# Kernel optimization log

Measured on AMD Instinct MI355X. Metric: run time of the kernel, lower is better.

Reference implementation:

```python
import jax, jax.numpy as jnp
import numpy as np
from jax import lax

DILATIONS = [1, 2, 4, 8, 16, 32, 64, 128, 256, 512]
L = len(DILATIONS)
T = 2048          # input_size (== sequence length)
C = 128           # residual channels
COND = 16         # condition vector dim
B = 8


def conv1d(x, w, dilation=1):
    # x: [B, T, Cin], w: [K, Cin, Cout] (WIO), SAME padding like keras Conv1D
    return lax.conv_general_dilated(
        x, w, window_strides=(1,), padding='SAME',
        rhs_dilation=(dilation,), dimension_numbers=('NWC', 'WIO', 'NWC'))


def setup_inputs() -> dict:
    key = jax.random.key(0)
    ks = iter(jax.random.split(key, 32))
    n = lambda shape, s=0.05: jax.random.normal(next(ks), shape, dtype=jnp.float32) * s
    inp = {
        'x': jax.random.normal(next(ks), (B, T, 1), dtype=jnp.float32),
        'condition': jax.random.normal(next(ks), (B, COND), dtype=jnp.float32),
        # input projection Conv1D(128, 1)
        'Wc': n((1, 1, C)), 'bc': jnp.zeros((C,), jnp.float32),
        # per-block dilated gated convs Conv1D(128, 3), stacked over L blocks
        'Wt': n((L, 3, C, C)), 'bt': jnp.zeros((L, C), jnp.float32),
        'Ws': n((L, 3, C, C)), 'bs': jnp.zeros((L, C), jnp.float32),
        # stacked conditioning Dense weights: 128 Dense(cond->T) per branch per block
        # Dense i weight [COND, T]; stacked & transposed -> [L, COND, T, 128]
        'Dt': n((L, COND, T, C)), 'Bt': jnp.zeros((L, T, C), jnp.float32),
        'Ds': n((L, COND, T, C)), 'Bs': jnp.zeros((L, T, C), jnp.float32),
        # skip / residual 1x1 convs
        'Wskip': n((L, 1, C, C)), 'bskip': jnp.zeros((L, C), jnp.float32),
        'Wres': n((L, 1, C, C)), 'bres': jnp.zeros((L, C), jnp.float32),
        # output head
        'W1': n((3, C, 2048)), 'b1': jnp.zeros((2048,), jnp.float32),
        'W2': n((3, 2048, 256)), 'b2': jnp.zeros((256,), jnp.float32),
        'W3': n((1, 256, 1)), 'b3': jnp.zeros((1,), jnp.float32),
    }
    return inp


def reference(x, condition, Wc, bc, Wt, bt, Ws, bs, Dt, Bt, Ds, Bs,
              Wskip, bskip, Wres, bres, W1, b1, W2, b2, W3, b3):
    h = conv1d(x, Wc) + bc  # [B, T, 128]
    skip_sum = jnp.zeros_like(h)
    for l, d in enumerate(DILATIONS):
        # fused equivalent of 128 per-channel Dense layers + concat:
        # trans[b,t,k] = condition[b,:] @ Dense_k.W + Dense_k.b
        tt = jnp.einsum('bc,ctk->btk', condition, Dt[l]) + Bt[l]
        ts = jnp.einsum('bc,ctk->btk', condition, Ds[l]) + Bs[l]
        g = jnp.tanh(conv1d(h, Wt[l], d) + bt[l] + tt) * \
            jax.nn.sigmoid(conv1d(h, Ws[l], d) + bs[l] + ts)
        skip_sum = skip_sum + conv1d(g, Wskip[l]) + bskip[l]
        h = conv1d(g, Wres[l]) + bres[l] + h
    out = jax.nn.relu(conv1d(skip_sum, W1) + b1)  # [B, T, 2048]
    out = jax.nn.relu(conv1d(out, W2) + b2)       # [B, T, 256]
    out = jnp.tanh(conv1d(out, W3) + b3)          # [B, T, 1]
    return out
```

## Files before the change

kernel.cpp:

```cpp
#include <hip/hip_runtime.h>
#include <hip/hip_bf16.h>
#include <math.h>

#define T 2048
#define C 128
#define BATCH 8
#define NLAYER 10

typedef short bf16x8 __attribute__((ext_vector_type(8)));
typedef float f32x4 __attribute__((ext_vector_type(4)));
typedef unsigned short u16x4 __attribute__((ext_vector_type(4)));

__device__ __forceinline__ float sigmoidf_(float x) {
    return 1.f / (1.f + __expf(-x));
}
__device__ __forceinline__ float tanhf_(float x) {
    float a = fabsf(x);
    float e = __expf(-2.f * a);
    float t = (1.f - e) / (1.f + e);
    return copysignf(t, x);
}
__device__ __forceinline__ ushort f2bf(float v) {
    __hip_bfloat16 h = __float2bfloat16(v);
    return *reinterpret_cast<ushort*>(&h);
}
__device__ __forceinline__ float bf2f(ushort u) {
    unsigned int x = ((unsigned int)u) << 16;
    return __uint_as_float(x);
}
__device__ __forceinline__ void gl_lds16(const ushort* g, ushort* l) {
    __builtin_amdgcn_global_load_lds(
        (const __attribute__((address_space(1))) unsigned int*)g,
        (__attribute__((address_space(3))) unsigned int*)l, 16, 0, 0);
}

__global__ void k_init(const float* __restrict__ x, const float* __restrict__ Wc,
                       const float* __restrict__ bc, float* __restrict__ h32,
                       ushort* __restrict__ hb, float* __restrict__ skip) {
    int i = blockIdx.x * 256 + threadIdx.x;
    int c = i & 127;
    int pos = i >> 7;
    float v = x[pos] * Wc[c] + bc[c];
    h32[i] = v;
    hb[i] = f2bf(v);
    skip[i] = 0.f;
}

__global__ void k_prep_wg(const float* __restrict__ Wt, const float* __restrict__ Ws,
                          ushort* __restrict__ WGb) {
    int n = blockIdx.x;
    int l = blockIdx.y;
    int t = threadIdx.x;
    int j = t >> 7, ci = t & 127;
    const float* src = (n < 128) ? Wt : Ws;
    int col = n & 127;
    WGb[((size_t)(l * 256 + n)) * 384 + t] = f2bf(src[(((size_t)l * 3 + j) * 128 + ci) * 128 + col]);
}
__global__ void k_prep_wr(const float* __restrict__ Wskip, const float* __restrict__ Wres,
                          ushort* __restrict__ WRb) {
    int n = blockIdx.x;
    int l = blockIdx.y;
    int ci = threadIdx.x;
    const float* src = (n < 128) ? Wskip : Wres;
    int col = n & 127;
    WRb[((size_t)(l * 256 + n)) * 128 + ci] = f2bf(src[((size_t)l * 128 + ci) * 128 + col]);
}
template<int KIN>
__global__ void k_prep_w(const float* __restrict__ W, ushort* __restrict__ Wb, int N) {
    int n = blockIdx.x;
    for (int k = threadIdx.x; k < 3 * KIN; k += blockDim.x)
        Wb[(size_t)n * (3 * KIN) + k] = f2bf(W[(size_t)k * N + n]);
}
__global__ void k_f32_to_bf16(const float* __restrict__ in, ushort* __restrict__ out, int n) {
    int i = blockIdx.x * 256 + threadIdx.x;
    if (i < n) out[i] = f2bf(in[i]);
}
__global__ void k_zero_pad(ushort* __restrict__ out1p) {
    int i = blockIdx.x * 256 + threadIdx.x;
    int ri = i >> 10, col = i & 1023;
    int b = ri >> 1, pr = (ri & 1) ? 2049 : 0;
    ((unsigned int*)out1p)[((size_t)b * 2050 + pr) * 1024 + col] = 0u;
}

__global__ __launch_bounds__(256) void k_cond(
    const float* __restrict__ cond,
    const float* __restrict__ Dt, const float* __restrict__ Bt,
    const float* __restrict__ Ds, const float* __restrict__ Bs,
    const float* __restrict__ bt, const float* __restrict__ bs,
    ushort* __restrict__ z0, int l0)
{
    const int l  = l0 + blockIdx.y;
    const int ll = blockIdx.y;
    const int k4 = (threadIdx.x & 31) * 4;
    const int tq = threadIdx.x >> 5;
    const int t  = blockIdx.x * 8 + tq;

    __shared__ float sc[128];
    if (threadIdx.x < 128) sc[threadIdx.x] = cond[threadIdx.x];
    __syncthreads();

    const f32x4 btv = *(const f32x4*)(bt + l * 128 + k4);
    const f32x4 bsv = *(const f32x4*)(bs + l * 128 + k4);
    const f32x4 Btv = *(const f32x4*)(Bt + ((size_t)l * T + t) * 128 + k4);
    const f32x4 Bsv = *(const f32x4*)(Bs + ((size_t)l * T + t) * 128 + k4);

    f32x4 zt[8], zs[8];
    #pragma unroll
    for (int b = 0; b < 8; ++b) {
        zt[b] = btv + Btv;
        zs[b] = bsv + Bsv;
    }

    const float* dtp = Dt + (((size_t)l * 16) * T + t) * 128 + k4;
    const float* dsp = Ds + (((size_t)l * 16) * T + t) * 128 + k4;
    #pragma unroll
    for (int c = 0; c < 16; ++c) {
        const f32x4 dv = *(const f32x4*)(dtp + (size_t)c * T * 128);
        const f32x4 sv = *(const f32x4*)(dsp + (size_t)c * T * 128);
        #pragma unroll
        for (int b = 0; b < 8; ++b) {
            const float cb = sc[b * 16 + c];
            zt[b] += cb * dv;
            zs[b] += cb * sv;
        }
    }

    #pragma unroll
    for (int b = 0; b < 8; ++b) {
        size_t zb = (((size_t)ll * 8 + b) * T + t) * 256;
        u16x4 pt, ps;
        #pragma unroll
        for (int j = 0; j < 4; ++j) {
            pt[j] = f2bf(zt[b][j]);
            ps[j] = f2bf(zs[b][j]);
        }
        *(u16x4*)(z0 + zb + k4)       = pt;
        *(u16x4*)(z0 + zb + 128 + k4) = ps;
    }
}

__global__ __launch_bounds__(256) void k_gate(
    const float* __restrict__ h32_in, float* __restrict__ h32_out,
    const ushort* __restrict__ hb_in, ushort* __restrict__ hb_out,
    float* __restrict__ skip32,
    const ushort* __restrict__ WG,
    const ushort* __restrict__ WR,
    const ushort* __restrict__ z0l,
    const float* __restrict__ bskip, const float* __restrict__ bres,
    int d)
{
    __shared__ ushort lds[3 * 32 * 136];
    const int tid  = threadIdx.x;
    const int lane = tid & 63, ln16 = lane & 15, quad = lane >> 4;
    const int wave = tid >> 6;
    const int n_off = wave * 64;
    const int t0 = blockIdx.x * 4;

    #pragma unroll
    for (int it = 0; it < 6; ++it) {
        int task = tid + it * 256;
        int part = task & 15;
        int r = (task >> 4) & 31;
        int j = task >> 9;
        int t = t0 + (r >> 3) + (j - 1) * d;
        int b = r & 7;
        uint4 v = make_uint4(0u, 0u, 0u, 0u);
        if (t >= 0 && t < T) v = *(const uint4*)(hb_in + ((size_t)b * T + t) * 128 + part * 8);
        *(uint4*)(&lds[(j * 32 + r) * 136 + part * 8]) = v;
    }
    __syncthreads();

    f32x4 acc[2][4];
    #pragma unroll
    for (int mt = 0; mt < 2; ++mt)
        #pragma unroll
        for (int nt = 0; nt < 4; ++nt)
            acc[mt][nt] = (f32x4){0.f, 0.f, 0.f, 0.f};

    #pragma unroll
    for (int j = 0; j < 3; ++j) {
        #pragma unroll
        for (int kc = 0; kc < 4; ++kc) {
            bf16x8 af[2], bfr[4];
            #pragma unroll
            for (int mt = 0; mt < 2; ++mt)
                af[mt] = *(const bf16x8*)(&lds[(j * 32 + mt * 16 + ln16) * 136 + kc * 32 + quad * 8]);
            #pragma unroll
            for (int nt = 0; nt < 4; ++nt)
                bfr[nt] = *(const bf16x8*)(WG + (size_t)(n_off + nt * 16 + ln16) * 384 + j * 128 + kc * 32 + quad * 8);
            #pragma unroll
            for (int mt = 0; mt < 2; ++mt)
                #pragma unroll
                for (int nt = 0; nt < 4; ++nt)
                    acc[mt][nt] = __builtin_amdgcn_mfma_f32_16x16x32_bf16(af[mt], bfr[nt], acc[mt][nt], 0, 0, 0);
        }
    }
    __syncthreads();

    #pragma unroll
    for (int mt = 0; mt < 2; ++mt) {
        #pragma unroll
        for (int nt = 0; nt < 4; ++nt) {
            int n = n_off + nt * 16 + ln16;
            #pragma unroll
            for (int r4 = 0; r4 < 4; ++r4) {
                int row = mt * 16 + quad * 4 + r4;
                int b = row & 7, p = row >> 3;
                float z = acc[mt][nt][r4] + bf2f(z0l[((size_t)b * T + t0 + p) * 256 + n]);
                lds[row * 264 + n] = f2bf(z);
            }
        }
    }
    __syncthreads();

    {
        int r = tid >> 3;
        int k0 = (tid & 7) * 16;
        #pragma unroll
        for (int kk = 0; kk < 16; ++kk) {
            int k = k0 + kk;
            float zt = bf2f(lds[r * 264 + k]);
            float zs = bf2f(lds[r * 264 + 128 + k]);
            lds[8704 + r * 136 + k] = f2bf(tanhf_(zt) * sigmoidf_(zs));
        }
    }
    __syncthreads();

    f32x4 acc2[2][4];
    #pragma unroll
    for (int mt = 0; mt < 2; ++mt)
        #pragma unroll
        for (int nt = 0; nt < 4; ++nt)
            acc2[mt][nt] = (f32x4){0.f, 0.f, 0.f, 0.f};

    #pragma unroll
    for (int kc = 0; kc < 4; ++kc) {
        bf16x8 af[2], bfr[4];
        #pragma unroll
        for (int mt = 0; mt < 2; ++mt)
            af[mt] = *(const bf16x8*)(&lds[8704 + (mt * 16 + ln16) * 136 + kc * 32 + quad * 8]);
        #pragma unroll
        for (int nt = 0; nt < 4; ++nt)
            bfr[nt] = *(const bf16x8*)(WR + (size_t)(n_off + nt * 16 + ln16) * 128 + kc * 32 + quad * 8);
        #pragma unroll
        for (int mt = 0; mt < 2; ++mt)
            #pragma unroll
            for (int nt = 0; nt < 4; ++nt)
                acc2[mt][nt] = __builtin_amdgcn_mfma_f32_16x16x32_bf16(af[mt], bfr[nt], acc2[mt][nt], 0, 0, 0);
    }

    #pragma unroll
    for (int mt = 0; mt < 2; ++mt) {
        #pragma unroll
        for (int nt = 0; nt < 4; ++nt) {
            int n = n_off + nt * 16 + ln16;
            int k = n & 127;
            #pragma unroll
            for (int r4 = 0; r4 < 4; ++r4) {
                int row = mt * 16 + quad * 4 + r4;
                int b = row & 7, p = row >> 3;
                size_t idx = ((size_t)b * T + t0 + p) * 128 + k;
                float v = acc2[mt][nt][r4];
                if (n < 128) {
                    skip32[idx] += v + bskip[k];
                } else {
                    float hv = v + bres[k] + h32_in[idx];
                    h32_out[idx] = hv;
                    hb_out[idx] = f2bf(hv);
                }
            }
        }
    }
}

template<int KIN, bool OUT_BF16>
__global__ __launch_bounds__(256) void k_conv_mfma(
    const ushort* __restrict__ A, const ushort* __restrict__ Wb,
    const float* __restrict__ bias, void* __restrict__ outv,
    int b_in_off, int b_out_off, int ots, int oto)
{
    constexpr int AS = 40;
    __shared__ ushort As[66 * AS];
    __shared__ ushort Bs[3 * 128 * AS];

    const int tid  = threadIdx.x;
    const int lane = tid & 63;
    const int ln16 = lane & 15;
    const int quad = lane >> 4;
    const int wave = tid >> 6;
    const int m_off = (wave & 1) * 32;
    const int n_off = (wave >> 1) * 64;

    const int t0 = blockIdx.x * 64;
    const int n0 = blockIdx.y * 128;
    const int bz = blockIdx.z;
    const int N  = gridDim.y * 128;

    const ushort* Ab = A + (size_t)(b_in_off + bz) * T * KIN;

    f32x4 acc[2][4];
    #pragma unroll
    for (int mi = 0; mi < 2; ++mi)
        #pragma unroll
        for (int ni = 0; ni < 4; ++ni)
            acc[mi][ni] = (f32x4){0.f, 0.f, 0.f, 0.f};

    for (int cc = 0; cc < KIN / 32; ++cc) {
        for (int idx = tid; idx < 66 * 4; idx += 256) {
            int r = idx >> 2, part = idx & 3;
            int t = t0 - 1 + r;
            uint4 v = make_uint4(0u, 0u, 0u, 0u);
            if (t >= 0 && t < T)
                v = *(const uint4*)(Ab + (size_t)t * KIN + cc * 32 + part * 8);
            *(uint4*)(&As[r * AS + part * 8]) = v;
        }
        #pragma unroll
        for (int it = 0; it < 6; ++it) {
            int idx = tid + it * 256;
            int jr = idx >> 2, part = idx & 3;
            int j = jr >> 7, n = jr & 127;
            uint4 v = *(const uint4*)(Wb + (size_t)(n0 + n) * (3 * KIN) + j * KIN + cc * 32 + part * 8);
            *(uint4*)(&Bs[jr * AS + part * 8]) = v;
        }
        __syncthreads();

        #pragma unroll
        for (int j = 0; j < 3; ++j) {
            bf16x8 af[2], bf[4];
            #pragma unroll
            for (int mi = 0; mi < 2; ++mi)
                af[mi] = *(const bf16x8*)(&As[(m_off + mi * 16 + ln16 + j) * AS + quad * 8]);
            #pragma unroll
            for (int ni = 0; ni < 4; ++ni)
                bf[ni] = *(const bf16x8*)(&Bs[(j * 128 + n_off + ni * 16 + ln16) * AS + quad * 8]);
            #pragma unroll
            for (int mi = 0; mi < 2; ++mi)
                #pragma unroll
                for (int ni = 0; ni < 4; ++ni)
                    acc[mi][ni] = __builtin_amdgcn_mfma_f32_16x16x32_bf16(af[mi], bf[ni], acc[mi][ni], 0, 0, 0);
        }
        __syncthreads();
    }

    #pragma unroll
    for (int ni = 0; ni < 4; ++ni) {
        int n = n0 + n_off + ni * 16 + ln16;
        float bv = bias[n];
        #pragma unroll
        for (int mi = 0; mi < 2; ++mi) {
            #pragma unroll
            for (int r = 0; r < 4; ++r) {
                int m = m_off + mi * 16 + quad * 4 + r;
                int t = t0 + m;
                float v = fmaxf(acc[mi][ni][r] + bv, 0.f);
                size_t oi = ((size_t)(b_out_off + bz) * ots + oto + t) * N + n;
                if constexpr (OUT_BF16) ((ushort*)outv)[oi] = f2bf(v);
                else                    ((float*)outv)[oi]  = v;
            }
        }
    }
}

#define CV2_AUS 8704
#define CV2_BUS 24576
#define CV2_BUF 33280

__global__ __launch_bounds__(256) void k_conv2t(
    const ushort* __restrict__ A,
    const ushort* __restrict__ Wb,
    const float* __restrict__ bias,
    float* __restrict__ out2)
{
    __shared__ ushort sh[2 * CV2_BUF];
    const int tid  = threadIdx.x;
    const int lane = tid & 63, ln16 = lane & 15, quad = lane >> 4;
    const int wave = tid >> 6;
    const int wm = wave >> 1, wn = wave & 1;
    const int m0 = blockIdx.x * 128;
    const int b  = blockIdx.y;
    const int n0 = blockIdx.z * 128;
    const size_t aRow0 = (size_t)b * 2050 + m0;

    f32x4 acc[4][4];
    #pragma unroll
    for (int i = 0; i < 4; ++i)
        #pragma unroll
        for (int j = 0; j < 4; ++j) acc[i][j] = (f32x4){0.f, 0.f, 0.f, 0.f};

    auto stage = [&](int d, int cc) {
        const int sb = d * CV2_BUF;
        const int k0 = cc * 64;
        #pragma unroll
        for (int ps = 0; ps < 4; ++ps) {
            int task = ps * 256 + tid;
            int r = task >> 3, p = task & 7, q = p ^ (r & 7);
            gl_lds16(A + (aRow0 + r) * 2048 + k0 + q * 8,
                     &sh[sb + ((ps * 256 + wave * 64) << 3)]);
        }
        if (tid < 64) {
            int task = 1024 + tid;
            int r = task >> 3, p = task & 7, q = p ^ (r & 7);
            gl_lds16(A + (aRow0 + r) * 2048 + k0 + q * 8,
                     &sh[sb + (1024 << 3)]);
        }
        #pragma unroll
        for (int ps = 0; ps < 12; ++ps) {
            int task = ps * 256 + tid;
            int rb = task >> 3, p = task & 7, q = p ^ (rb & 7);
            int nl = rb & 127, tap = rb >> 7;
            gl_lds16(Wb + (size_t)(n0 + nl) * 6144 + tap * 2048 + k0 + q * 8,
                     &sh[sb + CV2_AUS + ((ps * 256 + wave * 64) << 3)]);
        }
    };

    stage(0, 0);
    __syncthreads();

    for (int cc = 0; cc < 32; ++cc) {
        if (cc < 31) stage((cc + 1) & 1, cc + 1);
        const int sb = (cc & 1) * CV2_BUF;
        #pragma unroll
        for (int j = 0; j < 3; ++j) {
            #pragma unroll
            for (int kk = 0; kk < 2; ++kk) {
                bf16x8 af[4], bfr[4];
                #pragma unroll
                for (int mt = 0; mt < 4; ++mt) {
                    int r = wm * 64 + mt * 16 + ln16 + j;
                    int s = (kk << 2) | quad;
                    af[mt] = *(const bf16x8*)(&sh[sb + r * 64 + ((s ^ (r & 7)) << 3)]);
                }
                #pragma unroll
                for (int nt = 0; nt < 4; ++nt) {
                    int rb = j * 128 + wn * 64 + nt * 16 + ln16;
                    int s = (kk << 2) | quad;
                    bfr[nt] = *(const bf16x8*)(&sh[sb + CV2_AUS + rb * 64 + ((s ^ (rb & 7)) << 3)]);
                }
                #pragma unroll
                for (int mt = 0; mt < 4; ++mt)
                    #pragma unroll
                    for (int nt = 0; nt < 4; ++nt)
                        acc[mt][nt] = __builtin_amdgcn_mfma_f32_16x16x32_bf16(af[mt], bfr[nt], acc[mt][nt], 0, 0, 0);
            }
        }
        __syncthreads();
    }

    #pragma unroll
    for (int nt = 0; nt < 4; ++nt) {
        int n = n0 + wn * 64 + nt * 16 + ln16;
        float bv = bias[n];
        #pragma unroll
        for (int mt = 0; mt < 4; ++mt) {
            #pragma unroll
            for (int r4 = 0; r4 < 4; ++r4) {
                int m = wm * 64 + mt * 16 + quad * 4 + r4;
                int t = m0 + m;
                float v = fmaxf(acc[mt][nt][r4] + bv, 0.f);
                out2[((size_t)b * T + t) * 256 + n] = v;
            }
        }
    }
}

__global__ __launch_bounds__(256) void k_conv3(
    const float* __restrict__ out2, const float* __restrict__ W3,
    const float* __restrict__ b3, float* __restrict__ out)
{
    int wid = threadIdx.x >> 6, lane = threadIdx.x & 63;
    int pos = blockIdx.x * 4 + wid;
    float4 v = *(const float4*)(out2 + (size_t)pos * 256 + lane * 4);
    float4 w = *(const float4*)(W3 + lane * 4);
    float sum = v.x * w.x + v.y * w.y + v.z * w.z + v.w * w.w;
    #pragma unroll
    for (int off = 32; off > 0; off >>= 1) sum += __shfl_down(sum, off);
    if (lane == 0) out[pos] = tanhf_(sum + b3[0]);
}

extern "C" void kernel_launch(void* const* d_in, const int* in_sizes, int n_in,
                              void* d_out, int out_size, void* d_ws, size_t ws_size,
                              hipStream_t stream)
{
    const float* x     = (const float*)d_in[0];
    const float* cond  = (const float*)d_in[1];
    const float* Wc    = (const float*)d_in[2];
    const float* bc    = (const float*)d_in[3];
    const float* Wt    = (const float*)d_in[4];
    const float* bt    = (const float*)d_in[5];
    const float* Ws    = (const float*)d_in[6];
    const float* bs    = (const float*)d_in[7];
    const float* Dt    = (const float*)d_in[8];
    const float* Bt    = (const float*)d_in[9];
    const float* Ds    = (const float*)d_in[10];
    const float* Bs    = (const float*)d_in[11];
    const float* Wskip = (const float*)d_in[12];
    const float* bskip = (const float*)d_in[13];
    const float* Wres  = (const float*)d_in[14];
    const float* bres  = (const float*)d_in[15];
    const float* W1    = (const float*)d_in[16];
    const float* b1    = (const float*)d_in[17];
    const float* W2    = (const float*)d_in[18];
    const float* b2    = (const float*)d_in[19];
    const float* W3    = (const float*)d_in[20];
    const float* b3    = (const float*)d_in[21];
    float* out = (float*)d_out;

    float* ws = (float*)d_ws;
    float*  skip32 = ws;
    float*  h32a   = ws + 2097152;
    float*  h32b   = ws + 4194304;
    float*  out2   = ws + 6291456;
    ushort* u      = (ushort*)(ws + 10485760);
    ushort* hba    = u;
    ushort* hbb    = u + 2097152;
    ushort* WGb    = u + 4194304;
    ushort* WRb    = u + 5177344;
    ushort* W1b    = u + 5505024;
    ushort* W2b    = u + 6291456;
    ushort* skipb  = u;
    ushort* z0     = u + 9961472;
    ushort* out1p  = u + 7864320;

    k_init<<<8192, 256, 0, stream>>>(x, Wc, bc, h32a, hba, skip32);
    k_prep_wg<<<dim3(256, NLAYER), 384, 0, stream>>>(Wt, Ws, WGb);
    k_prep_wr<<<dim3(256, NLAYER), 128, 0, stream>>>(Wskip, Wres, WRb);
    k_prep_w<128><<<2048, 384, 0, stream>>>(W1, W1b, 2048);
    k_prep_w<2048><<<256, 1024, 0, stream>>>(W2, W2b, 256);

    static const int DIL[NLAYER] = {1, 2, 4, 8, 16, 32, 64, 128, 256, 512};
    float*  h32in = h32a;  float*  h32out = h32b;
    ushort* hbin  = hba;   ushort* hbout  = hbb;

    for (int chunk = 0; chunk < 2; ++chunk) {
        int l0 = chunk * 5;
        k_cond<<<dim3(T / 8, 5), 256, 0, stream>>>(cond, Dt, Bt, Ds, Bs, bt, bs, z0, l0);
        for (int l = l0; l < l0 + 5; ++l) {
            k_gate<<<512, 256, 0, stream>>>(
                h32in, h32out, hbin, hbout, skip32,
                WGb + (size_t)l * 256 * 384,
                WRb + (size_t)l * 256 * 128,
                z0 + (size_t)(l - l0) * 8 * T * 256,
                bskip + l * 128, bres + l * 128,
                DIL[l]);
            float* tf = h32in; h32in = h32out; h32out = tf;
            ushort* tu = hbin; hbin = hbout; hbout = tu;
        }
    }

    k_f32_to_bf16<<<(BATCH * T * C + 255) / 256, 256, 0, stream>>>(skip32, skipb, BATCH * T * C);
    k_zero_pad<<<64, 256, 0, stream>>>(out1p);
    k_conv_mfma<128, true><<<dim3(T / 64, 16, BATCH), 256, 0, stream>>>(
        skipb, W1b, b1, out1p, 0, 0, 2050, 1);
    k_conv2t<<<dim3(16, 8, 2), 256, 0, stream>>>(out1p, W2b, b2, out2);
    k_conv3<<<(BATCH * T) / 4, 256, 0, stream>>>(out2, W3, b3, out);
}
```

Baseline: 867.8 us.

## Tile weight prep transposes, split cond branches, rewrite conv1 with padded LDS-staged MFMA

Weight-prep kernels now transpose through 32x32 shared-memory tiles, so both global reads and writes are coalesced instead of strided. k_cond is split over a grid z-dimension into one block per branch (t/s), halving per-thread work and raising parallelism. The first head conv is replaced by a 128x128-tile MFMA kernel that reads a zero-padded skip buffer through direct global-to-LDS loads with XOR swizzle and double buffering, mirroring the conv2 kernel. Padding removes the boundary checks, at the cost of an extra padded layout and larger LDS use per block.

```diff
diff --git a/kernel.cpp b/kernel.cpp
--- a/kernel.cpp
+++ b/kernel.cpp
@@ -46,40 +46,72 @@
     skip[i] = 0.f;
 }
 
-__global__ void k_prep_wg(const float* __restrict__ Wt, const float* __restrict__ Ws,
-                          ushort* __restrict__ WGb) {
-    int n = blockIdx.x;
-    int l = blockIdx.y;
-    int t = threadIdx.x;
-    int j = t >> 7, ci = t & 127;
-    const float* src = (n < 128) ? Wt : Ws;
-    int col = n & 127;
-    WGb[((size_t)(l * 256 + n)) * 384 + t] = f2bf(src[(((size_t)l * 3 + j) * 128 + ci) * 128 + col]);
-}
-__global__ void k_prep_wr(const float* __restrict__ Wskip, const float* __restrict__ Wres,
-                          ushort* __restrict__ WRb) {
-    int n = blockIdx.x;
-    int l = blockIdx.y;
-    int ci = threadIdx.x;
-    const float* src = (n < 128) ? Wskip : Wres;
-    int col = n & 127;
-    WRb[((size_t)(l * 256 + n)) * 128 + ci] = f2bf(src[((size_t)l * 128 + ci) * 128 + col]);
-}
-template<int KIN>
-__global__ void k_prep_w(const float* __restrict__ W, ushort* __restrict__ Wb, int N) {
-    int n = blockIdx.x;
-    for (int k = threadIdx.x; k < 3 * KIN; k += blockDim.x)
-        Wb[(size_t)n * (3 * KIN) + k] = f2bf(W[(size_t)k * N + n]);
-}
-__global__ void k_f32_to_bf16(const float* __restrict__ in, ushort* __restrict__ out, int n) {
+__global__ void k_prep_wgT(const float* __restrict__ Wt, const float* __restrict__ Ws,
+                           ushort* __restrict__ WGb) {
+    const int tx = threadIdx.x, ty = threadIdx.y;
+    const int z = blockIdx.z, s = z & 1, lj = z >> 1;
+    const int l = lj / 3, j = lj % 3;
+    const float* src = (s ? Ws : Wt) + (size_t)lj * 128 * 128;
+    const int col0 = blockIdx.x * 32, ci0 = blockIdx.y * 32;
+    __shared__ float tile[32][33];
+    #pragma unroll
+    for (int i = 0; i < 4; ++i)
+        tile[ty + i * 8][tx] = src[(size_t)(ci0 + ty + i * 8) * 128 + col0 + tx];
+    __syncthreads();
+    #pragma unroll
+    for (int i = 0; i < 4; ++i)
+        WGb[((size_t)l * 256 + s * 128 + col0 + ty + i * 8) * 384 + j * 128 + ci0 + tx] =
+            f2bf(tile[tx][ty + i * 8]);
+}
+__global__ void k_prep_wrT(const float* __restrict__ Wskip, const float* __restrict__ Wres,
+                           ushort* __restrict__ WRb) {
+    const int tx = threadIdx.x, ty = threadIdx.y;
+    const int z = blockIdx.z, s = z & 1, l = z >> 1;
+    const float* src = (s ? Wres : Wskip) + (size_t)l * 128 * 128;
+    const int col0 = blockIdx.x * 32, ci0 = blockIdx.y * 32;
+    __shared__ float tile[32][33];
+    #pragma unroll
+    for (int i = 0; i < 4; ++i)
+        tile[ty + i * 8][tx] = src[(size_t)(ci0 + ty + i * 8) * 128 + col0 + tx];
+    __syncthreads();
+    #pragma unroll
+    for (int i = 0; i < 4; ++i)
+        WRb[((size_t)l * 256 + s * 128 + col0 + ty + i * 8) * 128 + ci0 + tx] =
+            f2bf(tile[tx][ty + i * 8]);
+}
+template<int R>
+__global__ void k_prep_wT(const float* __restrict__ W, ushort* __restrict__ Wb, int N) {
+    const int tx = threadIdx.x, ty = threadIdx.y;
+    const int x = blockIdx.x * 32 + tx;
+    const int y0 = blockIdx.y * 32;
+    __shared__ float tile[32][33];
+    #pragma unroll
+    for (int i = 0; i < 4; ++i)
+        tile[ty + i * 8][tx] = W[(size_t)(y0 + ty + i * 8) * N + x];
+    __syncthreads();
+    const int n0 = blockIdx.x * 32;
+    #pragma unroll
+    for (int i = 0; i < 4; ++i)
+        Wb[(size_t)(n0 + ty + i * 8) * R + y0 + tx] = f2bf(tile[tx][ty + i * 8]);
+}
+
+__global__ void k_skip_pad(const float* __restrict__ in, ushort* __restrict__ skipp) {
     int i = blockIdx.x * 256 + threadIdx.x;
-    if (i < n) out[i] = f2bf(in[i]);
-}
-__global__ void k_zero_pad(ushort* __restrict__ out1p) {
+    int b = i >> 18, rem = i & 262143;
+    skipp[(size_t)b * 262400 + 128 + rem] = f2bf(in[i]);
+}
+__global__ void k_zero_pads(ushort* __restrict__ out1p, ushort* __restrict__ skipp) {
     int i = blockIdx.x * 256 + threadIdx.x;
-    int ri = i >> 10, col = i & 1023;
-    int b = ri >> 1, pr = (ri & 1) ? 2049 : 0;
-    ((unsigned int*)out1p)[((size_t)b * 2050 + pr) * 1024 + col] = 0u;
+    if (i < 16384) {
+        int ri = i >> 10, col = i & 1023;
+        int b = ri >> 1, pr = (ri & 1) ? 2049 : 0;
+        ((unsigned int*)out1p)[((size_t)b * 2050 + pr) * 1024 + col] = 0u;
+    } else {
+        int j = i - 16384;
+        int ri = j >> 6, col = j & 63;
+        int b = ri >> 1, pr = (ri & 1) ? 2049 : 0;
+        ((unsigned int*)skipp)[((size_t)b * 2050 + pr) * 64 + col] = 0u;
+    }
 }
 
 __global__ __launch_bounds__(256) void k_cond(
@@ -89,6 +121,10 @@
     const float* __restrict__ bt, const float* __restrict__ bs,
     ushort* __restrict__ z0, int l0)
 {
+    const int br = blockIdx.z;
+    const float* D  = br ? Ds : Dt;
+    const float* B_ = br ? Bs : Bt;
+    const float* b_ = br ? bs : bt;
     const int l  = l0 + blockIdx.y;
     const int ll = blockIdx.y;
     const int k4 = (threadIdx.x & 31) * 4;
@@ -99,43 +135,29 @@
     if (threadIdx.x < 128) sc[threadIdx.x] = cond[threadIdx.x];
     __syncthreads();
 
-    const f32x4 btv = *(const f32x4*)(bt + l * 128 + k4);
-    const f32x4 bsv = *(const f32x4*)(bs + l * 128 + k4);
-    const f32x4 Btv = *(const f32x4*)(Bt + ((size_t)l * T + t) * 128 + k4);
-    const f32x4 Bsv = *(const f32x4*)(Bs + ((size_t)l * T + t) * 128 + k4);
-
-    f32x4 zt[8], zs[8];
-    #pragma unroll
-    for (int b = 0; b < 8; ++b) {
-        zt[b] = btv + Btv;
-        zs[b] = bsv + Bsv;
-    }
-
-    const float* dtp = Dt + (((size_t)l * 16) * T + t) * 128 + k4;
-    const float* dsp = Ds + (((size_t)l * 16) * T + t) * 128 + k4;
+    const f32x4 bv = *(const f32x4*)(b_ + l * 128 + k4);
+    const f32x4 Bv = *(const f32x4*)(B_ + ((size_t)l * T + t) * 128 + k4);
+
+    f32x4 z[8];
+    #pragma unroll
+    for (int b = 0; b < 8; ++b) z[b] = bv + Bv;
+
+    const float* dp = D + (((size_t)l * 16) * T + t) * 128 + k4;
     #pragma unroll
     for (int c = 0; c < 16; ++c) {
-        const f32x4 dv = *(const f32x4*)(dtp + (size_t)c * T * 128);
-        const f32x4 sv = *(const f32x4*)(dsp + (size_t)c * T * 128);
-        #pragma unroll
-        for (int b = 0; b < 8; ++b) {
-            const float cb = sc[b * 16 + c];
-            zt[b] += cb * dv;
-            zs[b] += cb * sv;
-        }
+        const f32x4 dv = *(const f32x4*)(dp + (size_t)c * T * 128);
+        #pragma unroll
+        for (int b = 0; b < 8; ++b)
+            z[b] += sc[b * 16 + c] * dv;
     }
 
     #pragma unroll
     for (int b = 0; b < 8; ++b) {
         size_t zb = (((size_t)ll * 8 + b) * T + t) * 256;
-        u16x4 pt, ps;
-        #pragma unroll
-        for (int j = 0; j < 4; ++j) {
-            pt[j] = f2bf(zt[b][j]);
-            ps[j] = f2bf(zs[b][j]);
-        }
-        *(u16x4*)(z0 + zb + k4)       = pt;
-        *(u16x4*)(z0 + zb + 128 + k4) = ps;
+        u16x4 p;
+        #pragma unroll
+        for (int j = 0; j < 4; ++j) p[j] = f2bf(z[b][j]);
+        *(u16x4*)(z0 + zb + br * 128 + k4) = p;
     }
 }
 
@@ -273,97 +295,106 @@
     }
 }
 
-template<int KIN, bool OUT_BF16>
-__global__ __launch_bounds__(256) void k_conv_mfma(
-    const ushort* __restrict__ A, const ushort* __restrict__ Wb,
-    const float* __restrict__ bias, void* __restrict__ outv,
-    int b_in_off, int b_out_off, int ots, int oto)
+#define CV2_AUS 8704
+#define CV2_BUF 33280
+
+__global__ __launch_bounds__(256) void k_conv1t(
+    const ushort* __restrict__ A,
+    const ushort* __restrict__ Wb,
+    const float* __restrict__ bias,
+    ushort* __restrict__ out1p)
 {
-    constexpr int AS = 40;
-    __shared__ ushort As[66 * AS];
-    __shared__ ushort Bs[3 * 128 * AS];
-
+    __shared__ ushort sh[2 * CV2_BUF];
     const int tid  = threadIdx.x;
-    const int lane = tid & 63;
-    const int ln16 = lane & 15;
-    const int quad = lane >> 4;
+    const int lane = tid & 63, ln16 = lane & 15, quad = lane >> 4;
     const int wave = tid >> 6;
-    const int m_off = (wave & 1) * 32;
-    const int n_off = (wave >> 1) * 64;
-
-    const int t0 = blockIdx.x * 64;
-    const int n0 = blockIdx.y * 128;
-    const int bz = blockIdx.z;
-    const int N  = gridDim.y * 128;
-
-    const ushort* Ab = A + (size_t)(b_in_off + bz) * T * KIN;
-
-    f32x4 acc[2][4];
-    #pragma unroll
-    for (int mi = 0; mi < 2; ++mi)
-        #pragma unroll
-        for (int ni = 0; ni < 4; ++ni)
-            acc[mi][ni] = (f32x4){0.f, 0.f, 0.f, 0.f};
-
-    for (int cc = 0; cc < KIN / 32; ++cc) {
-        for (int idx = tid; idx < 66 * 4; idx += 256) {
-            int r = idx >> 2, part = idx & 3;
-            int t = t0 - 1 + r;
-            uint4 v = make_uint4(0u, 0u, 0u, 0u);
-            if (t >= 0 && t < T)
-                v = *(const uint4*)(Ab + (size_t)t * KIN + cc * 32 + part * 8);
-            *(uint4*)(&As[r * AS + part * 8]) = v;
-        }
-        #pragma unroll
-        for (int it = 0; it < 6; ++it) {
-            int idx = tid + it * 256;
-            int jr = idx >> 2, part = idx & 3;
-            int j = jr >> 7, n = jr & 127;
-            uint4 v = *(const uint4*)(Wb + (size_t)(n0 + n) * (3 * KIN) + j * KIN + cc * 32 + part * 8);
-            *(uint4*)(&Bs[jr * AS + part * 8]) = v;
+    const int wm = wave >> 1, wn = wave & 1;
+    const int m0 = blockIdx.x * 128;
+    const int b  = blockIdx.y;
+    const int n0 = blockIdx.z * 128;
+    const size_t aRow0 = (size_t)b * 2050 + m0;
+
+    f32x4 acc[4][4];
+    #pragma unroll
+    for (int i = 0; i < 4; ++i)
+        #pragma unroll
+        for (int j = 0; j < 4; ++j) acc[i][j] = (f32x4){0.f, 0.f, 0.f, 0.f};
+
+    auto stage = [&](int d, int c) {
+        const int sb = d * CV2_BUF;
+        const int k0 = c * 64;
+        #pragma unroll
+        for (int ps = 0; ps < 4; ++ps) {
+            int task = ps * 256 + tid;
+            int r = task >> 3, p = task & 7, q = p ^ (r & 7);
+            gl_lds16(A + (aRow0 + r) * 128 + k0 + q * 8,
+                     &sh[sb + ((ps * 256 + wave * 64) << 3)]);
+        }
+        if (tid < 64) {
+            int task = 1024 + tid;
+            int r = task >> 3, p = task & 7, q = p ^ (r & 7);
+            gl_lds16(A + (aRow0 + r) * 128 + k0 + q * 8,
+                     &sh[sb + (1024 << 3)]);
+        }
+        #pragma unroll
+        for (int ps = 0; ps < 12; ++ps) {
+            int task = ps * 256 + tid;
+            int rb = task >> 3, p = task & 7, q = p ^ (rb & 7);
+            int nl = rb & 127, tap = rb >> 7;
+            gl_lds16(Wb + (size_t)(n0 + nl) * 384 + tap * 128 + k0 + q * 8,
+                     &sh[sb + CV2_AUS + ((ps * 256 + wave * 64) << 3)]);
+        }
+    };
+
+    stage(0, 0);
+    __syncthreads();
+
+    for (int c = 0; c < 2; ++c) {
+        if (c == 0) stage(1, 1);
+        const int sb = (c & 1) * CV2_BUF;
+        #pragma unroll
+        for (int j = 0; j < 3; ++j) {
+            #pragma unroll
+            for (int kk = 0; kk < 2; ++kk) {
+                bf16x8 af[4], bfr[4];
+                #pragma unroll
+                for (int mt = 0; mt < 4; ++mt) {
+                    int r = wm * 64 + mt * 16 + ln16 + j;
+                    int s = (kk << 2) | quad;
+                    af[mt] = *(const bf16x8*)(&sh[sb + r * 64 + ((s ^ (r & 7)) << 3)]);
+                }
+                #pragma unroll
+                for (int nt = 0; nt < 4; ++nt) {
+                    int rb = j * 128 + wn * 64 + nt * 16 + ln16;
+                    int s = (kk << 2) | quad;
+                    bfr[nt] = *(const bf16x8*)(&sh[sb + CV2_AUS + rb * 64 + ((s ^ (rb & 7)) << 3)]);
+                }
+                #pragma unroll
+                for (int mt = 0; mt < 4; ++mt)
+                    #pragma unroll
+                    for (int nt = 0; nt < 4; ++nt)
+                        acc[mt][nt] = __builtin_amdgcn_mfma_f32_16x16x32_bf16(af[mt], bfr[nt], acc[mt][nt], 0, 0, 0);
+            }
         }
         __syncthreads();
-
-        #pragma unroll
-        for (int j = 0; j < 3; ++j) {
-            bf16x8 af[2], bf[4];
-            #pragma unroll
-            for (int mi = 0; mi < 2; ++mi)
-                af[mi] = *(const bf16x8*)(&As[(m_off + mi * 16 + ln16 + j) * AS + quad * 8]);
-            #pragma unroll
-            for (int ni = 0; ni < 4; ++ni)
-                bf[ni] = *(const bf16x8*)(&Bs[(j * 128 + n_off + ni * 16 + ln16) * AS + quad * 8]);
-            #pragma unroll
-            for (int mi = 0; mi < 2; ++mi)
-                #pragma unroll
-                for (int ni = 0; ni < 4; ++ni)
-                    acc[mi][ni] = __builtin_amdgcn_mfma_f32_16x16x32_bf16(af[mi], bf[ni], acc[mi][ni], 0, 0, 0);
-        }
-        __syncthreads();
-    }
-
-    #pragma unroll
-    for (int ni = 0; ni < 4; ++ni) {
-        int n = n0 + n_off + ni * 16 + ln16;
+    }
+
+    #pragma unroll
+    for (int nt = 0; nt < 4; ++nt) {
+        int n = n0 + wn * 64 + nt * 16 + ln16;
         float bv = bias[n];
         #pragma unroll
-        for (int mi = 0; mi < 2; ++mi) {
-            #pragma unroll
-            for (int r = 0; r < 4; ++r) {
-                int m = m_off + mi * 16 + quad * 4 + r;
-                int t = t0 + m;
-                float v = fmaxf(acc[mi][ni][r] + bv, 0.f);
-                size_t oi = ((size_t)(b_out_off + bz) * ots + oto + t) * N + n;
-                if constexpr (OUT_BF16) ((ushort*)outv)[oi] = f2bf(v);
-                else                    ((float*)outv)[oi]  = v;
+        for (int mt = 0; mt < 4; ++mt) {
+            #pragma unroll
+            for (int r4 = 0; r4 < 4; ++r4) {
+                int m = wm * 64 + mt * 16 + quad * 4 + r4;
+                int t = m0 + m;
+                float v = fmaxf(acc[mt][nt][r4] + bv, 0.f);
+                out1p[((size_t)b * 2050 + 1 + t) * 2048 + n] = f2bf(v);
             }
         }
     }
 }
-
-#define CV2_AUS 8704
-#define CV2_BUS 24576
-#define CV2_BUF 33280
 
 __global__ __launch_bounds__(256) void k_conv2t(
     const ushort* __restrict__ A,
@@ -517,15 +548,15 @@
     ushort* WRb    = u + 5177344;
     ushort* W1b    = u + 5505024;
     ushort* W2b    = u + 6291456;
-    ushort* skipb  = u;
+    ushort* skipp  = u;
     ushort* z0     = u + 9961472;
     ushort* out1p  = u + 7864320;
 
     k_init<<<8192, 256, 0, stream>>>(x, Wc, bc, h32a, hba, skip32);
-    k_prep_wg<<<dim3(256, NLAYER), 384, 0, stream>>>(Wt, Ws, WGb);
-    k_prep_wr<<<dim3(256, NLAYER), 128, 0, stream>>>(Wskip, Wres, WRb);
-    k_prep_w<128><<<2048, 384, 0, stream>>>(W1, W1b, 2048);
-    k_prep_w<2048><<<256, 1024, 0, stream>>>(W2, W2b, 256);
+    k_prep_wgT<<<dim3(4, 4, 60), dim3(32, 8), 0, stream>>>(Wt, Ws, WGb);
+    k_prep_wrT<<<dim3(4, 4, 20), dim3(32, 8), 0, stream>>>(Wskip, Wres, WRb);
+    k_prep_wT<384><<<dim3(64, 12), dim3(32, 8), 0, stream>>>(W1, W1b, 2048);
+    k_prep_wT<6144><<<dim3(8, 192), dim3(32, 8), 0, stream>>>(W2, W2b, 256);
 
     static const int DIL[NLAYER] = {1, 2, 4, 8, 16, 32, 64, 128, 256, 512};
     float*  h32in = h32a;  float*  h32out = h32b;
@@ -533,7 +564,7 @@
 
     for (int chunk = 0; chunk < 2; ++chunk) {
         int l0 = chunk * 5;
-        k_cond<<<dim3(T / 8, 5), 256, 0, stream>>>(cond, Dt, Bt, Ds, Bs, bt, bs, z0, l0);
+        k_cond<<<dim3(T / 8, 5, 2), 256, 0, stream>>>(cond, Dt, Bt, Ds, Bs, bt, bs, z0, l0);
         for (int l = l0; l < l0 + 5; ++l) {
             k_gate<<<512, 256, 0, stream>>>(
                 h32in, h32out, hbin, hbout, skip32,
@@ -547,10 +578,9 @@
         }
     }
 
-    k_f32_to_bf16<<<(BATCH * T * C + 255) / 256, 256, 0, stream>>>(skip32, skipb, BATCH * T * C);
-    k_zero_pad<<<64, 256, 0, stream>>>(out1p);
-    k_conv_mfma<128, true><<<dim3(T / 64, 16, BATCH), 256, 0, stream>>>(
-        skipb, W1b, b1, out1p, 0, 0, 2050, 1);
+    k_skip_pad<<<8192, 256, 0, stream>>>(skip32, skipp);
+    k_zero_pads<<<68, 256, 0, stream>>>(out1p, skipp);
+    k_conv1t<<<dim3(16, 8, 16), 256, 0, stream>>>(skipp, W1b, b1, out1p);
     k_conv2t<<<dim3(16, 8, 2), 256, 0, stream>>>(out1p, W2b, b2, out2);
     k_conv3<<<(BATCH * T) / 4, 256, 0, stream>>>(out2, W3, b3, out);
 }
```

After: 868.5 us. Within noise of the previous version (+0.1%).
